# Optimization experiments

Hardware: AMD Instinct MI355X
Metric: run time of the kernel (lower is better)

## Reference

```python
import jax, jax.numpy as jnp
import numpy as np

EPS = 1e-6

def _rmsnorm(x, w):
    # normalize over last (head_dim) axis
    return x * jax.lax.rsqrt(jnp.mean(x * x, axis=-1, keepdims=True) + EPS) * w

def _rope(x, cos, sin):
    # x: [B, H, S, D]; cos/sin: [S, D]
    d = x.shape[-1]
    x1, x2 = x[..., : d // 2], x[..., d // 2 :]
    rot = jnp.concatenate([-x2, x1], axis=-1)
    return x * cos[None, None] + rot * sin[None, None]

def setup_inputs() -> dict:
    key = jax.random.key(0)
    B, S, D_MODEL = 1, 2048, 2048
    HEADS, HEAD_DIM, NKV = 32, 64, 8
    d_out = HEADS * HEAD_DIM
    kv_d_out = NKV * HEAD_DIM
    ks = jax.random.split(key, 8)
    x = jax.random.normal(ks[0], (B, S, D_MODEL), dtype=jnp.float32)
    # RoPE tables
    inv_freq = 1.0 / (10000.0 ** (jnp.arange(0, HEAD_DIM, 2, dtype=jnp.float32) / HEAD_DIM))
    pos = jnp.arange(S, dtype=jnp.float32)
    ang = pos[:, None] * inv_freq[None, :]            # [S, D/2]
    ang = jnp.concatenate([ang, ang], axis=-1)        # [S, D]
    sin, cos = jnp.sin(ang), jnp.cos(ang)
    mask = jnp.tril(jnp.ones((S, S), dtype=bool))     # causal: True = attend
    sd = 0.02
    Wq = jax.random.normal(ks[1], (D_MODEL, d_out), dtype=jnp.float32) * sd
    Wk = jax.random.normal(ks[2], (D_MODEL, kv_d_out), dtype=jnp.float32) * sd
    Wv = jax.random.normal(ks[3], (D_MODEL, kv_d_out), dtype=jnp.float32) * sd
    Wo = jax.random.normal(ks[4], (d_out, D_MODEL), dtype=jnp.float32) * sd
    bo = jnp.zeros((D_MODEL,), dtype=jnp.float32)
    q_scale = jnp.ones((HEAD_DIM,), dtype=jnp.float32)
    k_scale = jnp.ones((HEAD_DIM,), dtype=jnp.float32)
    return {"x": x, "sin": sin, "cos": cos, "mask": mask, "Wq": Wq, "Wk": Wk,
            "Wv": Wv, "Wo": Wo, "bo": bo, "q_scale": q_scale, "k_scale": k_scale}

def reference(x, sin, cos, mask, Wq, Wk, Wv, Wo, bo, q_scale, k_scale):
    B, S, _ = x.shape
    HEADS, HEAD_DIM, NKV = 32, 64, 8
    GS = HEADS // NKV  # group size = 4
    q = (x @ Wq).reshape(B, S, HEADS, HEAD_DIM).transpose(0, 2, 1, 3)  # [B,H,S,D]
    k = (x @ Wk).reshape(B, S, NKV, HEAD_DIM).transpose(0, 2, 1, 3)    # [B,G,S,D]
    v = (x @ Wv).reshape(B, S, NKV, HEAD_DIM).transpose(0, 2, 1, 3)    # [B,G,S,D]
    q = _rmsnorm(q, q_scale)
    k = _rmsnorm(k, k_scale)
    q = _rope(q, cos, sin)
    k = _rope(k, cos, sin)
    # GQA without materializing repeated k/v: group query heads per kv group
    qg = q.reshape(B, NKV, GS, S, HEAD_DIM)
    scale = 1.0 / jnp.sqrt(jnp.asarray(HEAD_DIM, dtype=x.dtype))
    scores = jnp.einsum('bghqd,bgkd->bghqk', qg, k) * scale  # [B,G,Gs,S,S]
    scores = jnp.where(mask[None, None, None], scores, jnp.asarray(-jnp.inf, dtype=scores.dtype))
    attn = jax.nn.softmax(scores, axis=-1)
    out = jnp.einsum('bghqk,bgkd->bghqd', attn, v)            # [B,G,Gs,S,D]
    out = out.reshape(B, HEADS, S, HEAD_DIM).transpose(0, 2, 1, 3).reshape(B, S, HEADS * HEAD_DIM)
    return out @ Wo + bo
```

## Files before the change

### kernel.cpp

```cpp
#include <hip/hip_runtime.h>
#include <stdint.h>


typedef __bf16 bf16x8 __attribute__((ext_vector_type(8)));
typedef __bf16 bf16x4v __attribute__((ext_vector_type(4)));
typedef float f32x4 __attribute__((ext_vector_type(4)));

#define MFMA_BF16(a, b, c) __builtin_amdgcn_mfma_f32_16x16x32_bf16(a, b, c, 0, 0, 0)

#if __has_builtin(__builtin_amdgcn_exp2f)
#define EXP2F(x) __builtin_amdgcn_exp2f(x)
#else
#define EXP2F(x) __expf((x) * 0.69314718055994531f)
#endif

#define QSCALE 0.18033688011112042f
#define SHIFT2 11.541560327111707f

__device__ __forceinline__ unsigned short f2bf(float f) {
  unsigned int u = __float_as_uint(f);
  u += 0x7fffu + ((u >> 16) & 1u);
  return (unsigned short)(u >> 16);
}

__device__ __forceinline__ void gload_lds16(const unsigned short* gsrc,
                                            unsigned short* ldst) {
  __builtin_amdgcn_global_load_lds(
      (const __attribute__((address_space(1))) unsigned int*)gsrc,
      (__attribute__((address_space(3))) unsigned int*)ldst, 16, 0, 0);
}

__global__ __launch_bounds__(256) void transpose_all(const float* __restrict__ Wq,
                                                     const float* __restrict__ Wk,
                                                     const float* __restrict__ Wv,
                                                     const float* __restrict__ Wo,
                                                     const float* __restrict__ x,
                                                     unsigned short* __restrict__ Wqkvt,
                                                     unsigned short* __restrict__ Wot,
                                                     unsigned short* __restrict__ xb) {
  int bx = blockIdx.x;
  int tid = threadIdx.x;
  if (bx >= 80) {
    int bid = (bx - 80) * 32 + blockIdx.y;
#pragma unroll
    for (int p = 0; p < 8; p++) {
      int i = bid * 8192 + p * 1024 + tid * 4;
      float4 v = *(const float4*)&x[i];
      ushort4 o;
      o.x = f2bf(v.x); o.y = f2bf(v.y); o.z = f2bf(v.z); o.w = f2bf(v.w);
      *(ushort4*)&xb[i] = o;
    }
    return;
  }
  const float* W;
  unsigned short* T;
  int N, nb;
  if (bx < 32)      { W = Wq; T = Wqkvt;                       N = 2048; nb = bx * 64; }
  else if (bx < 40) { W = Wk; T = Wqkvt + 2048 * 2048;         N = 512;  nb = (bx - 32) * 64; }
  else if (bx < 48) { W = Wv; T = Wqkvt + (size_t)2560 * 2048; N = 512;  nb = (bx - 40) * 64; }
  else              { W = Wo; T = Wot;                         N = 2048; nb = (bx - 48) * 64; }
  int kb = blockIdx.y * 64;
  __shared__ float tile[64][65];
#pragma unroll
  for (int i = 0; i < 16; i++) {
    int idx = tid + i * 256;
    int r = idx >> 6, c = idx & 63;
    tile[r][c] = W[(size_t)(kb + r) * N + nb + c];
  }
  __syncthreads();
#pragma unroll
  for (int i = 0; i < 8; i++) {
    int idx = tid + i * 256;
    int r = idx >> 5, cp = idx & 31;
    ushort2 o;
    o.x = f2bf(tile[2 * cp][r]);
    o.y = f2bf(tile[2 * cp + 1][r]);
    *(ushort2*)&T[(size_t)(nb + r) * 2048 + kb + 2 * cp] = o;
  }
}

#define GEMM_DBUF(A_, B_, m0_, n0_)                                            \
  int quad = lane >> 4, l16 = lane & 15;                                       \
  int wrow = (w & 1) * 32, wcol = (w >> 1) * 64;                               \
  int rsub = lane >> 3, csub = lane & 7;                                       \
  int chunk = csub ^ rsub;                                                     \
  int slotL = quad ^ (l16 & 7);                                                \
  const unsigned short* gA = &A_[(size_t)(m0_ + w * 16 + rsub) * 2048 + chunk * 8]; \
  const unsigned short* gB = &B_[(size_t)(n0_ + w * 32 + rsub) * 2048 + chunk * 8]; \
  int laOff = (w * 16) * 64 + lane * 8;                                        \
  int lbOff = 64 * 64 + (w * 32) * 64 + lane * 8;                              \
  f32x4 acc[2][4];                                                             \
  _Pragma("unroll") for (int i = 0; i < 2; i++)                                \
      _Pragma("unroll") for (int j = 0; j < 4; j++)                            \
          acc[i][j] = (f32x4){0.f, 0.f, 0.f, 0.f};                             \
  {                                                                            \
    unsigned short* sp = &Stage[0][0];                                         \
    gload_lds16(gA, sp + laOff);                                               \
    gload_lds16(gA + 8 * 2048, sp + laOff + 8 * 64);                           \
    gload_lds16(gB, sp + lbOff);                                               \
    gload_lds16(gB + 8 * 2048, sp + lbOff + 8 * 64);                           \
    gload_lds16(gB + 16 * 2048, sp + lbOff + 16 * 64);                         \
    gload_lds16(gB + 24 * 2048, sp + lbOff + 24 * 64);                         \
  }                                                                            \
  for (int k0 = 0; k0 < 2048; k0 += 64) {                                      \
    __syncthreads();                                                           \
    const unsigned short* cur = &Stage[(k0 >> 6) & 1][0];                      \
    unsigned short* nxt = &Stage[((k0 >> 6) + 1) & 1][0];                      \
    if (k0 + 64 < 2048) {                                                      \
      int kn = k0 + 64;                                                        \
      gload_lds16(gA + kn, nxt + laOff);                                       \
      gload_lds16(gA + 8 * 2048 + kn, nxt + laOff + 8 * 64);                   \
      gload_lds16(gB + kn, nxt + lbOff);                                       \
      gload_lds16(gB + 8 * 2048 + kn, nxt + lbOff + 8 * 64);                   \
      gload_lds16(gB + 16 * 2048 + kn, nxt + lbOff + 16 * 64);                 \
      gload_lds16(gB + 24 * 2048 + kn, nxt + lbOff + 24 * 64);                 \
    }                                                                          \
    const unsigned short* As = cur;                                            \
    const unsigned short* Bs = cur + 64 * 64;                                  \
    bf16x8 af[2][2], bfr[4][2];                                                \
    _Pragma("unroll") for (int i = 0; i < 2; i++) {                            \
      int base = (wrow + i * 16 + l16) * 64;                                   \
      af[i][0] = *(const bf16x8*)&As[base + slotL * 8];                        \
      af[i][1] = *(const bf16x8*)&As[base + (slotL ^ 4) * 8];                  \
    }                                                                          \
    _Pragma("unroll") for (int j = 0; j < 4; j++) {                            \
      int base = (wcol + j * 16 + l16) * 64;                                   \
      bfr[j][0] = *(const bf16x8*)&Bs[base + slotL * 8];                       \
      bfr[j][1] = *(const bf16x8*)&Bs[base + (slotL ^ 4) * 8];                 \
    }                                                                          \
    _Pragma("unroll") for (int kc = 0; kc < 2; kc++)                           \
        _Pragma("unroll") for (int i = 0; i < 2; i++)                          \
            _Pragma("unroll") for (int j = 0; j < 4; j++)                      \
                acc[i][j] = MFMA_BF16(af[i][kc], bfr[j][kc], acc[i][j]);       \
  }

__global__ __launch_bounds__(256, 3) void gemm_qkv(const unsigned short* __restrict__ A,
                                                   const unsigned short* __restrict__ B,
                                                   const float* __restrict__ sinp,
                                                   const float* __restrict__ cosp,
                                                   const float* __restrict__ q_scale,
                                                   const float* __restrict__ k_scale,
                                                   unsigned short* __restrict__ qh,
                                                   unsigned short* __restrict__ kh,
                                                   unsigned short* __restrict__ vt) {
  __shared__ __align__(16) unsigned short Stage[2][192 * 64];
  int tid = threadIdx.x;
  int w = tid >> 6, lane = tid & 63;
  int m0 = blockIdx.y * 64;
  int n0 = blockIdx.x * 128;
  GEMM_DBUF(A, B, m0, n0)

  int hd = blockIdx.x * 2 + (w >> 1);
  if (hd < 40) {
    const float* scl = (hd < 32) ? q_scale : k_scale;
    float wsc[4];
#pragma unroll
    for (int j = 0; j < 4; j++) wsc[j] = scl[j * 16 + l16];
    float oscale = (hd < 32) ? QSCALE : 1.0f;
#pragma unroll
    for (int i = 0; i < 2; i++)
#pragma unroll
      for (int r = 0; r < 4; r++) {
        float ss = 0.f;
#pragma unroll
        for (int j = 0; j < 4; j++) ss += acc[i][j][r] * acc[i][j][r];
#pragma unroll
        for (int off = 8; off; off >>= 1) ss += __shfl_xor(ss, off);
        float inv = rsqrtf(ss * (1.f / 64.f) + 1e-6f);
        int s = m0 + wrow + i * 16 + quad * 4 + r;
        float xn[4];
#pragma unroll
        for (int j = 0; j < 4; j++) xn[j] = acc[i][j][r] * inv * wsc[j];
#pragma unroll
        for (int j = 0; j < 4; j++) {
          int d = j * 16 + l16;
          float rot = (j < 2) ? -xn[j + 2] : xn[j - 2];
          float out = (xn[j] * cosp[s * 64 + d] + rot * sinp[s * 64 + d]) * oscale;
          if (hd < 32) qh[(size_t)s * 2048 + hd * 64 + d] = f2bf(out);
          else         kh[(size_t)s * 512 + (hd - 32) * 64 + d] = f2bf(out);
        }
      }
  } else {
    int g = hd - 40;
#pragma unroll
    for (int i = 0; i < 2; i++) {
      int t = (wrow + i * 16) >> 4;
      int slotb = (t & 1) * 32 + quad * 8 + (t >> 1) * 4;
#pragma unroll
      for (int j = 0; j < 4; j++) {
        bf16x4v pk;
#pragma unroll
        for (int r = 0; r < 4; r++) pk[r] = (__bf16)acc[i][j][r];
        *(bf16x4v*)&vt[(size_t)(g * 64 + j * 16 + l16) * 2048 + m0 + slotb] = pk;
      }
    }
  }
}

__global__ __launch_bounds__(256, 3) void gemm_out(const unsigned short* __restrict__ A,
                                                   const unsigned short* __restrict__ B,
                                                   float* __restrict__ C,
                                                   const float* __restrict__ bias) {
  __shared__ __align__(16) unsigned short Stage[2][192 * 64];
  int tid = threadIdx.x;
  int w = tid >> 6, lane = tid & 63;
  int m0 = blockIdx.y * 64;
  int n0 = blockIdx.x * 128;
  GEMM_DBUF(A, B, m0, n0)

#pragma unroll
  for (int i = 0; i < 2; i++) {
    int row = m0 + wrow + i * 16 + quad * 4;
#pragma unroll
    for (int j = 0; j < 4; j++) {
      int col = n0 + wcol + j * 16 + l16;
      float b = bias[col];
#pragma unroll
      for (int r = 0; r < 4; r++)
        C[(size_t)(row + r) * 2048 + col] = acc[i][j][r] + b;
    }
  }
}

__global__ __launch_bounds__(256, 4) void attention(const unsigned short* __restrict__ qh,
                                                    const unsigned short* __restrict__ kh,
                                                    const unsigned short* __restrict__ vt,
                                                    unsigned short* __restrict__ aout) {
  int h = blockIdx.y;
  int g = h >> 2;
  int tile = (blockIdx.x + blockIdx.y) & 31;
  int q0 = tile * 64;
  int w = threadIdx.x >> 6;
  int lane = threadIdx.x & 63;
  int quad = lane >> 4;
  int l16 = lane & 15;
  int qrow0 = q0 + w * 16;

  __shared__ __align__(16) unsigned short Stage[2][8192];

  int rsub = lane >> 3;
  int csub = lane & 7;
  int chunk = csub ^ rsub;

  const unsigned short* kg = &kh[(size_t)(w * 16 + rsub) * 512 + g * 64 + chunk * 8];
  const unsigned short* vg = &vt[(size_t)(g * 64 + w * 16 + rsub) * 2048 + chunk * 8];
  int klOff = (w * 16) * 64 + lane * 8;
  int vlOff = 4096 + (w * 16) * 64 + lane * 8;

  int posL = quad ^ (l16 & 7);
  int fL = l16 * 64 + posL * 8;
  int fH = l16 * 64 + (posL ^ 4) * 8;

  bf16x8 bq0 = *(const bf16x8*)&qh[(size_t)(qrow0 + l16) * 2048 + h * 64 + quad * 8];
  bf16x8 bq1 = *(const bf16x8*)&qh[(size_t)(qrow0 + l16) * 2048 + h * 64 + 32 + quad * 8];

  f32x4 o[4];
#pragma unroll
  for (int j = 0; j < 4; j++) o[j] = (f32x4){0.f, 0.f, 0.f, 0.f};
  float l_run = 0.f;

  int T = tile + 1;
  for (int it = 0; it < T; it += 2) {
    bool two = (it + 1 < T);
    __syncthreads();
    {
      int n0 = it << 6;
      unsigned short* sp = &Stage[0][0];
      gload_lds16(kg + (size_t)n0 * 512, sp + klOff);
      gload_lds16(kg + (size_t)(n0 + 8) * 512, sp + klOff + 8 * 64);
      gload_lds16(vg + n0, sp + vlOff);
      gload_lds16(vg + n0 + 8 * 2048, sp + vlOff + 8 * 64);
      if (two) {
        int n1 = n0 + 64;
        unsigned short* sp1 = &Stage[1][0];
        gload_lds16(kg + (size_t)n1 * 512, sp1 + klOff);
        gload_lds16(kg + (size_t)(n1 + 8) * 512, sp1 + klOff + 8 * 64);
        gload_lds16(vg + n1, sp1 + vlOff);
        gload_lds16(vg + n1 + 8 * 2048, sp1 + vlOff + 8 * 64);
      }
    }
    __syncthreads();

#pragma unroll
    for (int u = 0; u < 2; ++u) {
      if (u && !two) break;
      int itc = it + u;
      int n0 = itc << 6;
      const unsigned short* Ks = &Stage[u][0];
      const unsigned short* Vs = &Stage[u][4096];

      f32x4 s[4];
#pragma unroll
      for (int t = 0; t < 4; ++t) {
        bf16x8 kfl = *(const bf16x8*)&Ks[t * 1024 + fL];
        bf16x8 kfh = *(const bf16x8*)&Ks[t * 1024 + fH];
        f32x4 zz = (f32x4){0.f, 0.f, 0.f, 0.f};
        zz = MFMA_BF16(kfl, bq0, zz);
        s[t] = MFMA_BF16(kfh, bq1, zz);
      }

      float pv[4][4];
      if (itc == T - 1) {
        int qg = qrow0 + l16;
#pragma unroll
        for (int t = 0; t < 4; ++t)
#pragma unroll
          for (int r = 0; r < 4; ++r) {
            int key = n0 + t * 16 + quad * 4 + r;
            float p = (key <= qg) ? EXP2F(s[t][r] - SHIFT2) : 0.f;
            l_run += p;
            pv[t][r] = p;
          }
      } else {
#pragma unroll
        for (int t = 0; t < 4; ++t)
#pragma unroll
          for (int r = 0; r < 4; ++r) {
            float p = EXP2F(s[t][r] - SHIFT2);
            l_run += p;
            pv[t][r] = p;
          }
      }

      bf16x8 pf0, pf1;
#pragma unroll
      for (int j = 0; j < 4; ++j) {
        pf0[j] = (__bf16)pv[0][j];
        pf0[j + 4] = (__bf16)pv[2][j];
        pf1[j] = (__bf16)pv[1][j];
        pf1[j + 4] = (__bf16)pv[3][j];
      }

#pragma unroll
      for (int jd = 0; jd < 4; ++jd) {
        bf16x8 vfl = *(const bf16x8*)&Vs[jd * 1024 + fL];
        bf16x8 vfh = *(const bf16x8*)&Vs[jd * 1024 + fH];
        o[jd] = MFMA_BF16(vfl, pf0, o[jd]);
        o[jd] = MFMA_BF16(vfh, pf1, o[jd]);
      }
    }
  }

  l_run += __shfl_xor(l_run, 16);
  l_run += __shfl_xor(l_run, 32);
  float linv = 1.f / l_run;

  __syncthreads();
  unsigned short* Ob = &Stage[0][0] + w * (16 * 68);
#pragma unroll
  for (int jd = 0; jd < 4; ++jd) {
    bf16x4v pk;
#pragma unroll
    for (int r = 0; r < 4; ++r) pk[r] = (__bf16)(o[jd][r] * linv);
    *(bf16x4v*)&Ob[l16 * 68 + jd * 16 + quad * 4] = pk;
  }
  __threadfence_block();
#pragma unroll
  for (int rr = 0; rr < 2; ++rr) {
    int cidx = rr * 64 + lane;
    int row = cidx >> 3, ch = cidx & 7;
    bf16x8 v = *(const bf16x8*)&Ob[row * 68 + ch * 8];
    *(bf16x8*)&aout[(size_t)(qrow0 + row) * 2048 + h * 64 + ch * 8] = v;
  }
}

extern "C" void kernel_launch(void* const* d_in, const int* in_sizes, int n_in,
                              void* d_out, int out_size, void* d_ws, size_t ws_size,
                              hipStream_t stream) {
  (void)in_sizes; (void)n_in; (void)out_size; (void)ws_size;
  const float* x    = (const float*)d_in[0];
  const float* sinp = (const float*)d_in[1];
  const float* cosp = (const float*)d_in[2];
  const float* Wq = (const float*)d_in[4];
  const float* Wk = (const float*)d_in[5];
  const float* Wv = (const float*)d_in[6];
  const float* Wo = (const float*)d_in[7];
  const float* bo = (const float*)d_in[8];
  const float* q_scale = (const float*)d_in[9];
  const float* k_scale = (const float*)d_in[10];
  float* outp = (float*)d_out;

  uint8_t* ws = (uint8_t*)d_ws;
  const size_t MB = 1024 * 1024;
  unsigned short* xb    = (unsigned short*)(ws);
  unsigned short* Wqkvt = (unsigned short*)(ws + 8 * MB);
  unsigned short* Wot   = (unsigned short*)(ws + 20 * MB);
  unsigned short* qh    = (unsigned short*)(ws + 28 * MB);
  unsigned short* kh    = (unsigned short*)(ws + 36 * MB);
  unsigned short* vt    = (unsigned short*)(ws + 38 * MB);
  unsigned short* aout  = (unsigned short*)(ws + 40 * MB);

  transpose_all<<<dim3(96, 32), 256, 0, stream>>>(Wq, Wk, Wv, Wo, x, Wqkvt, Wot, xb);
  gemm_qkv<<<dim3(24, 32), 256, 0, stream>>>(xb, Wqkvt, sinp, cosp, q_scale, k_scale,
                                             qh, kh, vt);
  attention<<<dim3(32, 32), 256, 0, stream>>>(qh, kh, vt, aout);
  gemm_out<<<dim3(16, 32), 256, 0, stream>>>(aout, Wot, outp, bo);
}
```

Before: 205.8 us.

## Shrink out-projection tiles to 64x64 and rebalance causal attention tile order

The output projection GEMM moves from 64x128 tiles with the shared macro to a custom 64x64 tile kernel with an inline double-buffered LDS pipeline. This doubles the grid to 1024 blocks and raises the occupancy target to 4. The attention kernel's query-tile assignment now reverses order for alternating groups of heads so causal work is spread more evenly across CUs. Smaller GEMM tiles raise reuse overhead and global traffic per FLOP in exchange for more parallelism.

```diff
diff --git a/kernel.cpp b/kernel.cpp
--- a/kernel.cpp
+++ b/kernel.cpp
@@ -197,22 +197,73 @@
   }
 }
 
-__global__ __launch_bounds__(256, 3) void gemm_out(const unsigned short* __restrict__ A,
+__global__ __launch_bounds__(256, 4) void gemm_out(const unsigned short* __restrict__ A,
                                                    const unsigned short* __restrict__ B,
                                                    float* __restrict__ C,
                                                    const float* __restrict__ bias) {
-  __shared__ __align__(16) unsigned short Stage[2][192 * 64];
+  __shared__ __align__(16) unsigned short Stage[2][128 * 64];
   int tid = threadIdx.x;
   int w = tid >> 6, lane = tid & 63;
   int m0 = blockIdx.y * 64;
-  int n0 = blockIdx.x * 128;
-  GEMM_DBUF(A, B, m0, n0)
+  int n0 = blockIdx.x * 64;
+  int quad = lane >> 4, l16 = lane & 15;
+  int wrow = (w & 1) * 32, wcol = (w >> 1) * 32;
+  int rsub = lane >> 3, csub = lane & 7;
+  int chunk = csub ^ rsub;
+  int slotL = quad ^ (l16 & 7);
+  const unsigned short* gS = (w < 2)
+      ? &A[(size_t)(m0 + w * 32 + rsub) * 2048 + chunk * 8]
+      : &B[(size_t)(n0 + (w - 2) * 32 + rsub) * 2048 + chunk * 8];
+  int lsOff = (w * 32) * 64 + lane * 8;
+
+  f32x4 acc[2][2];
+#pragma unroll
+  for (int i = 0; i < 2; i++)
+#pragma unroll
+    for (int j = 0; j < 2; j++) acc[i][j] = (f32x4){0.f, 0.f, 0.f, 0.f};
+
+#pragma unroll
+  for (int c = 0; c < 4; c++)
+    gload_lds16(gS + (size_t)c * 8 * 2048, &Stage[0][0] + lsOff + c * 8 * 64);
+
+  for (int k0 = 0; k0 < 2048; k0 += 64) {
+    __syncthreads();
+    const unsigned short* cur = &Stage[(k0 >> 6) & 1][0];
+    unsigned short* nxt = &Stage[((k0 >> 6) + 1) & 1][0];
+    if (k0 + 64 < 2048) {
+#pragma unroll
+      for (int c = 0; c < 4; c++)
+        gload_lds16(gS + (size_t)c * 8 * 2048 + k0 + 64, nxt + lsOff + c * 8 * 64);
+    }
+    const unsigned short* As = cur;
+    const unsigned short* Bs = cur + 64 * 64;
+    bf16x8 af[2][2], bfr[2][2];
+#pragma unroll
+    for (int i = 0; i < 2; i++) {
+      int base = (wrow + i * 16 + l16) * 64;
+      af[i][0] = *(const bf16x8*)&As[base + slotL * 8];
+      af[i][1] = *(const bf16x8*)&As[base + (slotL ^ 4) * 8];
+    }
+#pragma unroll
+    for (int j = 0; j < 2; j++) {
+      int base = (wcol + j * 16 + l16) * 64;
+      bfr[j][0] = *(const bf16x8*)&Bs[base + slotL * 8];
+      bfr[j][1] = *(const bf16x8*)&Bs[base + (slotL ^ 4) * 8];
+    }
+#pragma unroll
+    for (int kc = 0; kc < 2; kc++)
+#pragma unroll
+      for (int i = 0; i < 2; i++)
+#pragma unroll
+        for (int j = 0; j < 2; j++)
+          acc[i][j] = MFMA_BF16(af[i][kc], bfr[j][kc], acc[i][j]);
+  }
 
 #pragma unroll
   for (int i = 0; i < 2; i++) {
     int row = m0 + wrow + i * 16 + quad * 4;
 #pragma unroll
-    for (int j = 0; j < 4; j++) {
+    for (int j = 0; j < 2; j++) {
       int col = n0 + wcol + j * 16 + l16;
       float b = bias[col];
 #pragma unroll
@@ -228,7 +279,8 @@
                                                     unsigned short* __restrict__ aout) {
   int h = blockIdx.y;
   int g = h >> 2;
-  int tile = (blockIdx.x + blockIdx.y) & 31;
+  int u = (blockIdx.x + (blockIdx.y & 7)) & 31;
+  int tile = ((blockIdx.y >> 3) & 1) ? (31 - u) : u;
   int q0 = tile * 64;
   int w = threadIdx.x >> 6;
   int lane = threadIdx.x & 63;
@@ -282,12 +334,12 @@
     __syncthreads();
 
 #pragma unroll
-    for (int u = 0; u < 2; ++u) {
-      if (u && !two) break;
-      int itc = it + u;
+    for (int uu = 0; uu < 2; ++uu) {
+      if (uu && !two) break;
+      int itc = it + uu;
       int n0 = itc << 6;
-      const unsigned short* Ks = &Stage[u][0];
-      const unsigned short* Vs = &Stage[u][4096];
+      const unsigned short* Ks = &Stage[uu][0];
+      const unsigned short* Vs = &Stage[uu][4096];
 
       f32x4 s[4];
 #pragma unroll
@@ -394,5 +446,5 @@
   gemm_qkv<<<dim3(24, 32), 256, 0, stream>>>(xb, Wqkvt, sinp, cosp, q_scale, k_scale,
                                              qh, kh, vt);
   attention<<<dim3(32, 32), 256, 0, stream>>>(qh, kh, vt, aout);
-  gemm_out<<<dim3(16, 32), 256, 0, stream>>>(aout, Wot, outp, bo);
-}
+  gemm_out<<<dim3(32, 32), 256, 0, stream>>>(aout, Wot, outp, bo);
+}
```

Result: slower. 216.9 us (+5.4%).
